# Kernel optimization log

Measured on AMD Instinct MI355X. Metric: run time of the kernel, lower is better.

Reference implementation:

```python
import jax, jax.numpy as jnp
import numpy as np

NUM_SPLITS = 4
SPLIT_CH = 4          # 16 channels / 4 splits
N_BRANCH = NUM_SPLITS * 2   # 2 pyramid branches per group
K = 2                 # multi_frequency_compression k
MAX_U, MAX_V = 5, 5
N_CLASSES = 60
LN_EPS = 1e-5


def _conv(x, w):
    # x: [B, Cin, H, W], w: [Cout, Cin, kh, kw], SAME padding, stride 1
    return jax.lax.conv_general_dilated(
        x, w, window_strides=(1, 1), padding='SAME',
        dimension_numbers=('NCHW', 'OIHW', 'NCHW'))


def _branch(x, w3, b3, w5, b5, w7, b7):
    # one PyramidMultiScaleCNN branch: dense 3x3 -> 5x5 -> 7x7 with input re-concat
    a = jax.nn.relu(_conv(x, w3) + b3[None, :, None, None])            # [B,64,H,W]
    b = jax.nn.relu(_conv(jnp.concatenate([a, x], 1), w5) + b5[None, :, None, None])  # [B,128,H,W]
    c = jax.nn.relu(_conv(jnp.concatenate([b, x], 1), w7) + b7[None, :, None, None])  # [B,256,H,W]
    return jnp.concatenate([a, b, c], axis=1)                          # [B,448,H,W]


def _dct_basis(H, W, dtype):
    # first K frequency pairs (u,v) in row-major order of a MAX_U x MAX_V grid
    uv = [(i // MAX_V, i % MAX_V) for i in range(K)]
    u = jnp.array([p[0] for p in uv], dtype=dtype)   # [K]
    v = jnp.array([p[1] for p in uv], dtype=dtype)   # [K]
    h = jnp.arange(H, dtype=dtype) + 0.5
    w = jnp.arange(W, dtype=dtype) + 0.5
    cos_u = jnp.cos(jnp.pi * u[:, None] * h[None, :] / H)  # [K,H]
    cos_v = jnp.cos(jnp.pi * v[:, None] * w[None, :] / W)  # [K,W]
    return cos_u, cos_v


def setup_inputs() -> dict:
    key = jax.random.key(0)
    ks = jax.random.split(key, 16)
    B, C, H, W = 16, 16, 32, 32
    s = 0.02
    x = jax.random.normal(ks[0], (B, C, H, W), jnp.float32)
    # stacked params for the 8 identical-shaped pyramid branches (index = 2*group + branch)
    w3 = jax.random.normal(ks[1], (N_BRANCH, 64, SPLIT_CH, 3, 3), jnp.float32) * s
    b3 = jnp.zeros((N_BRANCH, 64), jnp.float32)
    w5 = jax.random.normal(ks[2], (N_BRANCH, 128, 64 + SPLIT_CH, 5, 5), jnp.float32) * s
    b5 = jnp.zeros((N_BRANCH, 128), jnp.float32)
    w7 = jax.random.normal(ks[3], (N_BRANCH, 256, 128 + SPLIT_CH, 7, 7), jnp.float32) * s
    b7 = jnp.zeros((N_BRANCH, 256), jnp.float32)
    fused_c = N_BRANCH * 448  # 3584
    Wg = jax.random.normal(ks[4], (N_CLASSES, fused_c), jnp.float32) * s
    bg = jnp.zeros((N_CLASSES,), jnp.float32)
    f_dct = fused_c * K       # 7168
    gamma = jnp.ones((f_dct,), jnp.float32)
    beta = jnp.zeros((f_dct,), jnp.float32)
    Wd = jax.random.normal(ks[5], (N_CLASSES, f_dct), jnp.float32) * s
    bd = jnp.zeros((N_CLASSES,), jnp.float32)
    return {"x": x, "w3": w3, "b3": b3, "w5": w5, "b5": b5, "w7": w7, "b7": b7,
            "Wg": Wg, "bg": bg, "gamma": gamma, "beta": beta, "Wd": Wd, "bd": bd}


def reference(x, w3, b3, w5, b5, w7, b7, Wg, bg, gamma, beta, Wd, bd):
    B, C, H, W = x.shape
    # split channels into groups: [NUM_SPLITS, B, SPLIT_CH, H, W]
    parts = x.reshape(B, NUM_SPLITS, SPLIT_CH, H, W).transpose(1, 0, 2, 3, 4)
    # each group feeds 2 branches; branch index i = 2*group + branch matches fused cat order
    xg = jnp.repeat(parts, 2, axis=0)                               # [8,B,SPLIT_CH,H,W]
    outs = jax.vmap(_branch)(xg, w3, b3, w5, b5, w7, b7)            # [8,B,448,H,W]
    fused = outs.transpose(1, 0, 2, 3, 4).reshape(B, N_BRANCH * 448, H, W)  # [B,3584,H,W]

    # GAP head
    gap_feat = fused.mean(axis=(2, 3))                              # [B,3584]
    gap_pred = gap_feat @ Wg.T + bg                                 # [B,60]

    # batched multi-frequency DCT compression (replaces per-sample Python loop)
    cos_u, cos_v = _dct_basis(H, W, fused.dtype)                    # [K,H],[K,W]
    dct = jnp.einsum('bchw,kh,kw->bck', fused, cos_u, cos_v)        # [B,3584,K]
    dct = dct.reshape(B, -1)                                        # [B,7168]

    mu = dct.mean(axis=-1, keepdims=True)
    var = jnp.var(dct, axis=-1, keepdims=True)
    normed = (dct - mu) * jax.lax.rsqrt(var + LN_EPS) * gamma + beta
    # dropout omitted (eval mode)
    dct_pred = normed @ Wd.T + bd                                   # [B,60]
    return (gap_pred, dct_pred)
```

## Files before the change

kernel.cpp:

```cpp
#include <hip/hip_runtime.h>
#include <math.h>

#define PI_F 3.14159265358979323846f

typedef short bf16x8 __attribute__((ext_vector_type(8)));
typedef float f32x4  __attribute__((ext_vector_type(4)));

__device__ __forceinline__ short f2bf(float f) {
    union { float f; unsigned u; } v; v.f = f;
    unsigned r = v.u + 0x7fffu + ((v.u >> 16) & 1u);
    return (short)(r >> 16);
}


__global__ __launch_bounds__(256) void prep_s1in(const float* __restrict__ x, short* __restrict__ dst) {
    int idx = blockIdx.x * 256 + threadIdx.x;
    if (idx >= 64 * 1024) return;
    int px = idx & 1023;
    int g  = (idx >> 10) & 3;
    int b  = idx >> 12;
    short v8[8];
    #pragma unroll
    for (int j = 0; j < 8; ++j) {
        float f = (j < 4) ? x[((b * 16 + g * 4 + j) << 10) + px] : 0.f;
        v8[j] = f2bf(f);
    }
    *(int4*)(dst + (size_t)idx * 8) = *(const int4*)v8;
}

__global__ __launch_bounds__(256) void prep_sx(const float* __restrict__ x, short* __restrict__ dst,
                                               int CHS, int CH0) {
    int idx = blockIdx.x * 256 + threadIdx.x;
    if (idx >= 128 * 1024) return;
    int px = idx & 1023, pair = idx >> 10;
    int i = pair >> 4, b = pair & 15, g = i >> 1;
    short v8[8];
    #pragma unroll
    for (int j = 0; j < 8; ++j) {
        float f = (j < 4) ? x[((b * 16 + g * 4 + j) << 10) + px] : 0.f;
        v8[j] = f2bf(f);
    }
    *(int4*)(dst + (size_t)idx * CHS + CH0) = *(const int4*)v8;
}

template<int KS, int CHS, int CINR, int COUT, int NCH>
__global__ __launch_bounds__(256) void wprep_d(const float* __restrict__ w, short* __restrict__ Bw) {
    constexpr int TOTAL = 8 * KS * NCH * COUT * 4;
    int idx = blockIdx.x * 256 + threadIdx.x;
    if (idx >= TOTAL) return;
    int kb = idx & 3;
    int r  = idx >> 2;
    int n  = r % COUT;  r /= COUT;
    int c  = r % NCH;   r /= NCH;
    int kh = r % KS;
    int br = r / KS;
    short v8[8];
    #pragma unroll
    for (int j = 0; j < 8; ++j) {
        int k   = c * 32 + kb * 8 + j;
        int kwc = k / CHS;
        int ch  = k - kwc * CHS;
        float f = (kwc < KS && ch < CINR)
                ? w[(((size_t)br * COUT + n) * CINR + ch) * (KS * KS) + kh * KS + kwc] : 0.f;
        v8[j] = f2bf(f);
    }
    *(int4*)(Bw + (size_t)idx * 8) = *(const int4*)v8;
}

template<int KS, int CHS, int COUT, int CHS_OUT, int FOFF, bool S1SRC>
__global__ __launch_bounds__(512, 2) void conv_hk(
    const short* __restrict__ sIn,
    short* __restrict__ sOut,
    const short* __restrict__ Bw,
    const float* __restrict__ bias,
    float* __restrict__ sums)
{
    constexpr int PAD    = KS / 2;
    constexpr int NCH    = (KS * CHS + 31) / 32;
    constexpr int TCX    = 32 + (NCH * 32 - 1) / CHS;
    constexpr int NSLOT  = 9;
    constexpr int NFN    = COUT / 64;
    constexpr int CPP    = CHS / 8;
    constexpr int RCHK   = TCX * CPP;
    constexpr int CHUNKB = COUT * 32;
    static_assert(NCH == 1 || (NCH % 2) == 0, "NCH must be 1 or even");

    __shared__ int4 AtileV[(NSLOT * TCX * CHS) / 8];
    short* Atile = (short*)AtileV;

    const int t    = threadIdx.x;
    const int lane = t & 63, w = t >> 6;
    const int wm = w >> 2, wn = w & 3;
    const int lm = lane & 15, kb = lane >> 4;

    const int bid = blockIdx.x;
    const int i  = bid & 7;
    const int b  = (bid >> 3) & 15;
    const int mt = bid >> 7;
    const int r0 = mt * 8;

    const int pairPx = (i * 16 + b) << 10;
    const int srcPx  = S1SRC ? ((b * 4 + (i >> 1)) << 10) : pairPx;

    int nIdx[NFN], nOff[NFN];
    #pragma unroll
    for (int fn = 0; fn < NFN; ++fn) {
        nIdx[fn] = wn * (COUT / 4) + fn * 16 + lm;
        nOff[fn] = nIdx[fn] * 32 + kb * 8;
    }

    f32x4 acc[8][NFN];
    #pragma unroll
    for (int fm = 0; fm < 8; ++fm)
        #pragma unroll
        for (int fn = 0; fn < NFN; ++fn)
            acc[fm][fn] = (f32x4){0.f, 0.f, 0.f, 0.f};

    const short* Bp = Bw + (size_t)i * KS * NCH * CHUNKB;
    bf16x8 b0[NFN], b1[NFN];
    #pragma unroll
    for (int fn = 0; fn < NFN; ++fn)
        b0[fn] = *(const bf16x8*)(Bp + nOff[fn]);

    for (int e = t; e < 9 * RCHK; e += 512) {
        int j  = e / RCHK, e2 = e - j * RCHK;
        int tc = e2 / CPP, kc = e2 - tc * CPP;
        int rin = r0 - PAD + j, cin = tc - PAD;
        int4 v = {0, 0, 0, 0};
        if (rin >= 0 && rin < 32 && cin >= 0 && cin < 32)
            v = *(const int4*)(sIn + (size_t)(srcPx + rin * 32 + cin) * CHS + kc * 8);
        *(int4*)(Atile + (j * TCX + tc) * CHS + kc * 8) = v;
    }
    __syncthreads();

    for (int kh = 0; kh < KS; ++kh) {
        int aB[8];
        #pragma unroll
        for (int fm = 0; fm < 8; ++fm) {
            int slot = kh + wm * 4 + (fm >> 1);
            if (slot >= NSLOT) slot -= NSLOT;
            aB[fm] = (slot * TCX + (fm & 1) * 16 + lm) * CHS + kb * 8;
        }

        const bool doStage = (kh <= KS - 3);
        const int stRin = r0 - PAD + kh + 9;
        int4 stg0 = {0, 0, 0, 0}, stg1 = {0, 0, 0, 0};
        if (doStage) {
            if (t < RCHK) {
                int tc = t / CPP, kc = t - tc * CPP;
                int cin = tc - PAD;
                if (stRin >= 0 && stRin < 32 && cin >= 0 && cin < 32)
                    stg0 = *(const int4*)(sIn + (size_t)(srcPx + stRin * 32 + cin) * CHS + kc * 8);
            }
            if constexpr (RCHK > 512) {
                int e2 = t + 512;
                if (e2 < RCHK) {
                    int tc = e2 / CPP, kc = e2 - tc * CPP;
                    int cin = tc - PAD;
                    if (stRin >= 0 && stRin < 32 && cin >= 0 && cin < 32)
                        stg1 = *(const int4*)(sIn + (size_t)(srcPx + stRin * 32 + cin) * CHS + kc * 8);
                }
            }
        }

        if constexpr (NCH == 1) {
            __builtin_amdgcn_s_setprio(1);
            #pragma unroll
            for (int fm = 0; fm < 8; ++fm) {
                bf16x8 af = *(const bf16x8*)(Atile + aB[fm]);
                #pragma unroll
                for (int fn = 0; fn < NFN; ++fn)
                    acc[fm][fn] = __builtin_amdgcn_mfma_f32_16x16x32_bf16(af, b0[fn], acc[fm][fn], 0, 0, 0);
            }
            __builtin_amdgcn_s_setprio(0);
            if (kh < KS - 1) {
                #pragma unroll
                for (int fn = 0; fn < NFN; ++fn)
                    b0[fn] = *(const bf16x8*)(Bp + CHUNKB + nOff[fn]);
            }
            Bp += CHUNKB;
        } else {
            #pragma unroll 1
            for (int c = 0; c < NCH; c += 2) {
                #pragma unroll
                for (int fn = 0; fn < NFN; ++fn)
                    b1[fn] = *(const bf16x8*)(Bp + (size_t)(c + 1) * CHUNKB + nOff[fn]);
                __builtin_amdgcn_s_setprio(1);
                #pragma unroll
                for (int fm = 0; fm < 8; ++fm) {
                    bf16x8 af = *(const bf16x8*)(Atile + aB[fm] + c * 32);
                    #pragma unroll
                    for (int fn = 0; fn < NFN; ++fn)
                        acc[fm][fn] = __builtin_amdgcn_mfma_f32_16x16x32_bf16(af, b0[fn], acc[fm][fn], 0, 0, 0);
                }
                __builtin_amdgcn_s_setprio(0);
                if (!(kh == KS - 1 && c + 2 >= NCH)) {
                    #pragma unroll
                    for (int fn = 0; fn < NFN; ++fn)
                        b0[fn] = *(const bf16x8*)(Bp + (size_t)(c + 2) * CHUNKB + nOff[fn]);
                }
                __builtin_amdgcn_s_setprio(1);
                #pragma unroll
                for (int fm = 0; fm < 8; ++fm) {
                    bf16x8 af = *(const bf16x8*)(Atile + aB[fm] + (c + 1) * 32);
                    #pragma unroll
                    for (int fn = 0; fn < NFN; ++fn)
                        acc[fm][fn] = __builtin_amdgcn_mfma_f32_16x16x32_bf16(af, b1[fn], acc[fm][fn], 0, 0, 0);
                }
                __builtin_amdgcn_s_setprio(0);
            }
            Bp += (size_t)NCH * CHUNKB;
        }

        __syncthreads();
        if (doStage) {
            if (t < RCHK) {
                int tc = t / CPP, kc = t - tc * CPP;
                *(int4*)(Atile + (kh * TCX + tc) * CHS + kc * 8) = stg0;
            }
            if constexpr (RCHK > 512) {
                int e2 = t + 512;
                if (e2 < RCHK) {
                    int tc = e2 / CPP, kc = e2 - tc * CPP;
                    *(int4*)(Atile + (kh * TCX + tc) * CHS + kc * 8) = stg1;
                }
            }
        }
    }

    float cwv[2][4];
    #pragma unroll
    for (int half = 0; half < 2; ++half)
        #pragma unroll
        for (int r = 0; r < 4; ++r)
            cwv[half][r] = cosf(PI_F * (half * 16 + kb * 4 + r + 0.5f) / 32.f);

    #pragma unroll
    for (int fn = 0; fn < NFN; ++fn) {
        int n = nIdx[fn];
        float bv = bias[i * COUT + n];
        float s0 = 0.f, s1 = 0.f;
        #pragma unroll
        for (int fm = 0; fm < 8; ++fm) {
            int imgrow = wm * 4 + (fm >> 1);
            int half = fm & 1;
            #pragma unroll
            for (int r = 0; r < 4; ++r) {
                float v = fmaxf(acc[fm][fn][r] + bv, 0.f);
                if constexpr (CHS_OUT > 0) {
                    int col = half * 16 + kb * 4 + r;
                    int R = r0 + imgrow;
                    sOut[(size_t)(pairPx + R * 32 + col) * CHS_OUT + n] = f2bf(v);
                }
                s0 += v;
                s1 += v * cwv[half][r];
            }
        }
        s0 += __shfl_xor(s0, 16); s1 += __shfl_xor(s1, 16);
        s0 += __shfl_xor(s0, 32); s1 += __shfl_xor(s1, 32);
        if (kb == 0) {
            int ch = i * 448 + FOFF + n;
            atomicAdd(&sums[((size_t)b * 3584 + ch) * 2 + 0], s0);
            atomicAdd(&sums[((size_t)b * 3584 + ch) * 2 + 1], s1);
        }
    }
}

__global__ __launch_bounds__(256) void ln_stats(const float* __restrict__ sums,
                                                float* __restrict__ stats) {
    __shared__ float red[8];
    const int b = blockIdx.x;
    const int t = threadIdx.x, lane = t & 63, wv = t >> 6;
    const float* S = sums + (size_t)b * 7168;
    float ls = 0.f, lq = 0.f;
    for (int f = t; f < 7168; f += 256) { float v = S[f]; ls += v; lq += v * v; }
    for (int m = 1; m < 64; m <<= 1) { ls += __shfl_xor(ls, m); lq += __shfl_xor(lq, m); }
    if (lane == 0) { red[wv] = ls; red[4 + wv] = lq; }
    __syncthreads();
    if (t == 0) {
        float ts = red[0] + red[1] + red[2] + red[3];
        float tq = red[4] + red[5] + red[6] + red[7];
        float mu  = ts * (1.f / 7168.f);
        float var = tq * (1.f / 7168.f) - mu * mu;
        stats[b * 2 + 0] = mu;
        stats[b * 2 + 1] = rsqrtf(var + 1e-5f);
    }
}

__global__ __launch_bounds__(256) void head_gemv(
    const float* __restrict__ sums,
    const float* __restrict__ stats,
    const float* __restrict__ Wg, const float* __restrict__ bg,
    const float* __restrict__ gamma, const float* __restrict__ beta,
    const float* __restrict__ Wd, const float* __restrict__ bd,
    float* __restrict__ out)
{
    __shared__ float red[8];
    const int n = blockIdx.x % 60;
    const int b = blockIdx.x / 60;
    const int t = threadIdx.x, lane = t & 63, wv = t >> 6;
    const float* S  = sums + (size_t)b * 7168;
    const float mu  = stats[b * 2 + 0];
    const float inv = stats[b * 2 + 1];

    const float* wd = Wd + (size_t)n * 7168;
    float accd = 0.f;
    for (int f = t; f < 7168; f += 256) {
        float v = (S[f] - mu) * inv * gamma[f] + beta[f];
        accd = fmaf(v, wd[f], accd);
    }
    const float* wg = Wg + (size_t)n * 3584;
    float accg = 0.f;
    for (int ch = t; ch < 3584; ch += 256)
        accg = fmaf(S[2 * ch], wg[ch], accg);

    for (int m = 1; m < 64; m <<= 1) { accg += __shfl_xor(accg, m); accd += __shfl_xor(accd, m); }
    if (lane == 0) { red[wv] = accg; red[4 + wv] = accd; }
    __syncthreads();
    if (t == 0) {
        float g = red[0] + red[1] + red[2] + red[3];
        float d = red[4] + red[5] + red[6] + red[7];
        out[b * 60 + n]       = g * (1.f / 1024.f) + bg[n];
        out[960 + b * 60 + n] = d + bd[n];
    }
}

extern "C" void kernel_launch(void* const* d_in, const int* in_sizes, int n_in,
                              void* d_out, int out_size, void* d_ws, size_t ws_size,
                              hipStream_t stream)
{
    const float* x     = (const float*)d_in[0];
    const float* w3    = (const float*)d_in[1];
    const float* b3    = (const float*)d_in[2];
    const float* w5    = (const float*)d_in[3];
    const float* b5    = (const float*)d_in[4];
    const float* w7    = (const float*)d_in[5];
    const float* b7    = (const float*)d_in[6];
    const float* Wg    = (const float*)d_in[7];
    const float* bg    = (const float*)d_in[8];
    const float* gamma = (const float*)d_in[9];
    const float* beta  = (const float*)d_in[10];
    const float* Wd    = (const float*)d_in[11];
    const float* bd    = (const float*)d_in[12];
    float* out = (float*)d_out;

    char* p = (char*)d_ws;
    float* sums  = (float*)p;             p += 458752;
    float* stats = (float*)p;             p += 128;
    short* s1in = (short*)p;              p += 1048576;
    short* s2in = (short*)p;              p += 18874368;
    short* s3in = (short*)p;              p += 35651584;
    short* Bw3  = (short*)p;              p += 98304;
    short* Bw5  = (short*)p;              p += 3932160;
    short* Bw7  = (short*)p;              p += 27525120;

    hipMemsetAsync(sums, 0, 458752, stream);
    prep_s1in<<<dim3(256), dim3(256), 0, stream>>>(x, s1in);
    prep_sx<<<dim3(512), dim3(256), 0, stream>>>(x, s2in, 72, 64);
    prep_sx<<<dim3(512), dim3(256), 0, stream>>>(x, s3in, 136, 128);
    wprep_d<3, 8, 4, 64, 1><<<dim3(24), dim3(256), 0, stream>>>(w3, Bw3);
    wprep_d<5, 72, 68, 128, 12><<<dim3(960), dim3(256), 0, stream>>>(w5, Bw5);
    wprep_d<7, 136, 132, 256, 30><<<dim3(6720), dim3(256), 0, stream>>>(w7, Bw7);

    conv_hk<3, 8, 64, 72, 0, true><<<dim3(512), dim3(512), 0, stream>>>(s1in, s2in, Bw3, b3, sums);
    conv_hk<5, 72, 128, 136, 64, false><<<dim3(512), dim3(512), 0, stream>>>(s2in, s3in, Bw5, b5, sums);
    conv_hk<7, 136, 256, 0, 192, false><<<dim3(512), dim3(512), 0, stream>>>(s3in, nullptr, Bw7, b7, sums);

    ln_stats<<<dim3(16), dim3(256), 0, stream>>>(sums, stats);
    head_gemv<<<dim3(960), dim3(256), 0, stream>>>(sums, stats, Wg, bg, gamma, beta, Wd, bd, out);
}
```

Before: 493.0 us.

## Use 32x32x16 MFMA conv kernel with swizzled LDS for 5x5 and 7x7 layers

Adds a new conv kernel for the 5x5 and 7x7 layers that uses 32x32x16 bf16 MFMA tiles instead of 16x16x32. It restructures the per-wave M/N fragment mapping and epilogue, and applies an XOR swizzle to LDS addresses to reduce bank conflicts. The goal is fewer LDS reads and higher MFMA throughput per operand loaded. The trade-off is larger 16-wide accumulators, which raise register pressure. The old kernel drops its second staging path because it is now only used for the 3x3 layer.

```diff
diff --git a/kernel.cpp b/kernel.cpp
--- a/kernel.cpp
+++ b/kernel.cpp
@@ -5,6 +5,7 @@
 
 typedef short bf16x8 __attribute__((ext_vector_type(8)));
 typedef float f32x4  __attribute__((ext_vector_type(4)));
+typedef float f32x16 __attribute__((ext_vector_type(16)));
 
 __device__ __forceinline__ short f2bf(float f) {
     union { float f; unsigned u; } v; v.f = f;
@@ -144,7 +145,7 @@
 
         const bool doStage = (kh <= KS - 3);
         const int stRin = r0 - PAD + kh + 9;
-        int4 stg0 = {0, 0, 0, 0}, stg1 = {0, 0, 0, 0};
+        int4 stg0 = {0, 0, 0, 0};
         if (doStage) {
             if (t < RCHK) {
                 int tc = t / CPP, kc = t - tc * CPP;
@@ -152,15 +153,6 @@
                 if (stRin >= 0 && stRin < 32 && cin >= 0 && cin < 32)
                     stg0 = *(const int4*)(sIn + (size_t)(srcPx + stRin * 32 + cin) * CHS + kc * 8);
             }
-            if constexpr (RCHK > 512) {
-                int e2 = t + 512;
-                if (e2 < RCHK) {
-                    int tc = e2 / CPP, kc = e2 - tc * CPP;
-                    int cin = tc - PAD;
-                    if (stRin >= 0 && stRin < 32 && cin >= 0 && cin < 32)
-                        stg1 = *(const int4*)(sIn + (size_t)(srcPx + stRin * 32 + cin) * CHS + kc * 8);
-                }
-            }
         }
 
         if constexpr (NCH == 1) {
@@ -217,13 +209,6 @@
             if (t < RCHK) {
                 int tc = t / CPP, kc = t - tc * CPP;
                 *(int4*)(Atile + (kh * TCX + tc) * CHS + kc * 8) = stg0;
-            }
-            if constexpr (RCHK > 512) {
-                int e2 = t + 512;
-                if (e2 < RCHK) {
-                    int tc = e2 / CPP, kc = e2 - tc * CPP;
-                    *(int4*)(Atile + (kh * TCX + tc) * CHS + kc * 8) = stg1;
-                }
             }
         }
     }
@@ -259,6 +244,205 @@
         s0 += __shfl_xor(s0, 16); s1 += __shfl_xor(s1, 16);
         s0 += __shfl_xor(s0, 32); s1 += __shfl_xor(s1, 32);
         if (kb == 0) {
+            int ch = i * 448 + FOFF + n;
+            atomicAdd(&sums[((size_t)b * 3584 + ch) * 2 + 0], s0);
+            atomicAdd(&sums[((size_t)b * 3584 + ch) * 2 + 1], s1);
+        }
+    }
+}
+
+template<int KS, int CHS, int COUT, int CHS_OUT, int FOFF>
+__global__ __launch_bounds__(512, 2) void conv_hk32(
+    const short* __restrict__ sIn,
+    short* __restrict__ sOut,
+    const short* __restrict__ Bw,
+    const float* __restrict__ bias,
+    float* __restrict__ sums)
+{
+    constexpr int PAD    = KS / 2;
+    constexpr int NCH    = (KS * CHS + 31) / 32;
+    constexpr int TCX    = 32 + (NCH * 32 - 1) / CHS;
+    constexpr int NSLOT  = 9;
+    constexpr int NFN    = COUT / 128;
+    constexpr int CPP    = CHS / 8;
+    constexpr int RCHK   = TCX * CPP;
+    constexpr int CHUNKB = COUT * 32;
+    static_assert((NCH % 2) == 0, "NCH must be even");
+
+    __shared__ int4 AtileV[(NSLOT * TCX * CHS) / 8];
+    char* Alds = (char*)AtileV;
+
+    const int t    = threadIdx.x;
+    const int lane = t & 63, w = t >> 6;
+    const int wm = w >> 2, wn = w & 3;
+    const int ln = lane & 31, hi = lane >> 5;
+
+    const int bid = blockIdx.x;
+    const int i  = bid & 7;
+    const int b  = (bid >> 3) & 15;
+    const int mt = bid >> 7;
+    const int r0 = mt * 8;
+    const int pairPx = (i * 16 + b) << 10;
+
+    int nIdx[NFN], nOff[NFN];
+    #pragma unroll
+    for (int fn = 0; fn < NFN; ++fn) {
+        nIdx[fn] = wn * (COUT / 4) + fn * 32 + ln;
+        nOff[fn] = nIdx[fn] * 32 + hi * 8;
+    }
+
+    f32x16 acc[4][NFN];
+    #pragma unroll
+    for (int mf = 0; mf < 4; ++mf)
+        #pragma unroll
+        for (int fn = 0; fn < NFN; ++fn)
+            acc[mf][fn] = (f32x16)(0.f);
+
+    const short* Bp = Bw + (size_t)i * KS * NCH * CHUNKB;
+    bf16x8 b0[NFN][2], b1[NFN][2];
+    #pragma unroll
+    for (int fn = 0; fn < NFN; ++fn) {
+        b0[fn][0] = *(const bf16x8*)(Bp + nOff[fn]);
+        b0[fn][1] = *(const bf16x8*)(Bp + nOff[fn] + 16);
+    }
+
+    for (int e = t; e < 9 * RCHK; e += 512) {
+        int j  = e / RCHK, e2 = e - j * RCHK;
+        int tc = e2 / CPP, kc = e2 - tc * CPP;
+        int rin = r0 - PAD + j, cin = tc - PAD;
+        int4 v = {0, 0, 0, 0};
+        if (rin >= 0 && rin < 32 && cin >= 0 && cin < 32)
+            v = *(const int4*)(sIn + (size_t)(pairPx + rin * 32 + cin) * CHS + kc * 8);
+        int off = ((j * TCX + tc) * CHS + kc * 8) * 2;
+        off ^= ((off >> 7) & 1) << 4;
+        *(int4*)(Alds + off) = v;
+    }
+    __syncthreads();
+
+    for (int kh = 0; kh < KS; ++kh) {
+        int aB[4];
+        #pragma unroll
+        for (int mf = 0; mf < 4; ++mf) {
+            int slot = kh + wm * 4 + mf;
+            if (slot >= NSLOT) slot -= NSLOT;
+            aB[mf] = (slot * TCX + ln) * CHS * 2 + hi * 16;
+        }
+
+        const bool doStage = (kh <= KS - 3);
+        const int stRin = r0 - PAD + kh + 9;
+        int4 stg0 = {0, 0, 0, 0}, stg1 = {0, 0, 0, 0};
+        if (doStage) {
+            if (t < RCHK) {
+                int tc = t / CPP, kc = t - tc * CPP;
+                int cin = tc - PAD;
+                if (stRin >= 0 && stRin < 32 && cin >= 0 && cin < 32)
+                    stg0 = *(const int4*)(sIn + (size_t)(pairPx + stRin * 32 + cin) * CHS + kc * 8);
+            }
+            if constexpr (RCHK > 512) {
+                int e2 = t + 512;
+                if (e2 < RCHK) {
+                    int tc = e2 / CPP, kc = e2 - tc * CPP;
+                    int cin = tc - PAD;
+                    if (stRin >= 0 && stRin < 32 && cin >= 0 && cin < 32)
+                        stg1 = *(const int4*)(sIn + (size_t)(pairPx + stRin * 32 + cin) * CHS + kc * 8);
+                }
+            }
+        }
+
+        #pragma unroll 1
+        for (int c = 0; c < NCH; c += 2) {
+            #pragma unroll
+            for (int fn = 0; fn < NFN; ++fn) {
+                b1[fn][0] = *(const bf16x8*)(Bp + (size_t)(c + 1) * CHUNKB + nOff[fn]);
+                b1[fn][1] = *(const bf16x8*)(Bp + (size_t)(c + 1) * CHUNKB + nOff[fn] + 16);
+            }
+            __builtin_amdgcn_s_setprio(1);
+            #pragma unroll
+            for (int kk = 0; kk < 2; ++kk) {
+                #pragma unroll
+                for (int mf = 0; mf < 4; ++mf) {
+                    int off = aB[mf] + c * 64 + kk * 32;
+                    off ^= ((off >> 7) & 1) << 4;
+                    bf16x8 af = *(const bf16x8*)(Alds + off);
+                    #pragma unroll
+                    for (int fn = 0; fn < NFN; ++fn)
+                        acc[mf][fn] = __builtin_amdgcn_mfma_f32_32x32x16_bf16(af, b0[fn][kk], acc[mf][fn], 0, 0, 0);
+                }
+            }
+            __builtin_amdgcn_s_setprio(0);
+            if (!(kh == KS - 1 && c + 2 >= NCH)) {
+                #pragma unroll
+                for (int fn = 0; fn < NFN; ++fn) {
+                    b0[fn][0] = *(const bf16x8*)(Bp + (size_t)(c + 2) * CHUNKB + nOff[fn]);
+                    b0[fn][1] = *(const bf16x8*)(Bp + (size_t)(c + 2) * CHUNKB + nOff[fn] + 16);
+                }
+            }
+            __builtin_amdgcn_s_setprio(1);
+            #pragma unroll
+            for (int kk = 0; kk < 2; ++kk) {
+                #pragma unroll
+                for (int mf = 0; mf < 4; ++mf) {
+                    int off = aB[mf] + (c + 1) * 64 + kk * 32;
+                    off ^= ((off >> 7) & 1) << 4;
+                    bf16x8 af = *(const bf16x8*)(Alds + off);
+                    #pragma unroll
+                    for (int fn = 0; fn < NFN; ++fn)
+                        acc[mf][fn] = __builtin_amdgcn_mfma_f32_32x32x16_bf16(af, b1[fn][kk], acc[mf][fn], 0, 0, 0);
+                }
+            }
+            __builtin_amdgcn_s_setprio(0);
+        }
+        Bp += (size_t)NCH * CHUNKB;
+
+        __syncthreads();
+        if (doStage) {
+            if (t < RCHK) {
+                int tc = t / CPP, kc = t - tc * CPP;
+                int off = ((kh * TCX + tc) * CHS + kc * 8) * 2;
+                off ^= ((off >> 7) & 1) << 4;
+                *(int4*)(Alds + off) = stg0;
+            }
+            if constexpr (RCHK > 512) {
+                int e2 = t + 512;
+                if (e2 < RCHK) {
+                    int tc = e2 / CPP, kc = e2 - tc * CPP;
+                    int off = ((kh * TCX + tc) * CHS + kc * 8) * 2;
+                    off ^= ((off >> 7) & 1) << 4;
+                    *(int4*)(Alds + off) = stg1;
+                }
+            }
+        }
+    }
+
+    float cw[16];
+    #pragma unroll
+    for (int r = 0; r < 16; ++r) {
+        int px = (r & 3) + 8 * (r >> 2) + 4 * hi;
+        cw[r] = cosf(PI_F * (px + 0.5f) / 32.f);
+    }
+
+    #pragma unroll
+    for (int fn = 0; fn < NFN; ++fn) {
+        int n = nIdx[fn];
+        float bv = bias[i * COUT + n];
+        float s0 = 0.f, s1 = 0.f;
+        #pragma unroll
+        for (int mf = 0; mf < 4; ++mf) {
+            int R = r0 + wm * 4 + mf;
+            #pragma unroll
+            for (int r = 0; r < 16; ++r) {
+                float v = fmaxf(acc[mf][fn][r] + bv, 0.f);
+                if constexpr (CHS_OUT > 0) {
+                    int px = (r & 3) + 8 * (r >> 2) + 4 * hi;
+                    sOut[(size_t)(pairPx + R * 32 + px) * CHS_OUT + n] = f2bf(v);
+                }
+                s0 += v;
+                s1 += v * cw[r];
+            }
+        }
+        s0 += __shfl_xor(s0, 32);
+        s1 += __shfl_xor(s1, 32);
+        if (hi == 0) {
             int ch = i * 448 + FOFF + n;
             atomicAdd(&sums[((size_t)b * 3584 + ch) * 2 + 0], s0);
             atomicAdd(&sums[((size_t)b * 3584 + ch) * 2 + 1], s1);
@@ -363,8 +547,8 @@
     wprep_d<7, 136, 132, 256, 30><<<dim3(6720), dim3(256), 0, stream>>>(w7, Bw7);
 
     conv_hk<3, 8, 64, 72, 0, true><<<dim3(512), dim3(512), 0, stream>>>(s1in, s2in, Bw3, b3, sums);
-    conv_hk<5, 72, 128, 136, 64, false><<<dim3(512), dim3(512), 0, stream>>>(s2in, s3in, Bw5, b5, sums);
-    conv_hk<7, 136, 256, 0, 192, false><<<dim3(512), dim3(512), 0, stream>>>(s3in, nullptr, Bw7, b7, sums);
+    conv_hk32<5, 72, 128, 136, 64><<<dim3(512), dim3(512), 0, stream>>>(s2in, s3in, Bw5, b5, sums);
+    conv_hk32<7, 136, 256, 0, 192><<<dim3(512), dim3(512), 0, stream>>>(s3in, nullptr, Bw7, b7, sums);
 
     ln_stats<<<dim3(16), dim3(256), 0, stream>>>(sums, stats);
     head_gemv<<<dim3(960), dim3(256), 0, stream>>>(sums, stats, Wg, bg, gamma, beta, Wd, bd, out);
```

Result: slower. 516.5 us (+4.8%).
